# Kernel tuning notes

Hardware: AMD Instinct MI355X
Metric: run time of the kernel (lower is better)

Reference implementation:

```python
import jax, jax.numpy as jnp
import numpy as np

NEG = float(-2**32 + 1)  # padding value used by the original module
N_HEADS = 4


def setup_inputs() -> dict:
    key = jax.random.key(0)
    ks = jax.random.split(key, 12)
    B, L, H = 16, 200, 256
    queries = jax.random.normal(ks[0], (B, L, H), jnp.float32)
    keys = jax.random.normal(ks[1], (B, L, H), jnp.float32)
    time_mask = jax.random.randint(ks[2], (B, L), 0, 2) == 1
    attn_mask = jnp.triu(jnp.ones((L, L), dtype=bool), k=1)  # causal: True = masked
    time_matrix_K = jax.random.normal(ks[3], (B, L, L, H), jnp.float32) * 0.1
    time_matrix_V = jax.random.normal(ks[4], (B, L, L, H), jnp.float32) * 0.1
    abs_pos_K = jax.random.normal(ks[5], (B, L, H), jnp.float32)
    abs_pos_V = jax.random.normal(ks[6], (B, L, H), jnp.float32)
    s = 1.0 / np.sqrt(H)
    Wq = jax.random.normal(ks[7], (H, H), jnp.float32) * s
    Wk = jax.random.normal(ks[8], (H, H), jnp.float32) * s
    Wv = jax.random.normal(ks[9], (H, H), jnp.float32) * s
    bq = jnp.zeros((H,), jnp.float32)
    bk = jnp.zeros((H,), jnp.float32)
    bv = jnp.zeros((H,), jnp.float32)
    return dict(queries=queries, keys=keys, time_mask=time_mask, attn_mask=attn_mask,
                time_matrix_K=time_matrix_K, time_matrix_V=time_matrix_V,
                abs_pos_K=abs_pos_K, abs_pos_V=abs_pos_V,
                Wq=Wq, bq=bq, Wk=Wk, bk=bk, Wv=Wv, bv=bv)


def reference(queries, keys, time_mask, attn_mask, time_matrix_K, time_matrix_V,
              abs_pos_K, abs_pos_V, Wq, bq, Wk, bk, Wv, bv):
    B, L, H = queries.shape
    h = N_HEADS
    d = H // h
    # linear projections
    Q = (queries @ Wq.T + bq).reshape(B, L, h, d)
    K = (keys @ Wk.T + bk).reshape(B, L, h, d)
    V = (keys @ Wv.T + bv).reshape(B, L, h, d)
    posK = abs_pos_K.reshape(B, L, h, d)
    posV = abs_pos_V.reshape(B, L, h, d)
    tmK = time_matrix_K.reshape(B, L, L, h, d)
    tmV = time_matrix_V.reshape(B, L, L, h, d)
    # attention scores: content + absolute-position bias + per-row time bias
    scores = jnp.einsum('blhd,bmhd->bhlm', Q, K)
    scores += jnp.einsum('blhd,bmhd->bhlm', Q, posK)
    scores += jnp.einsum('blmhd,blhd->bhlm', tmK, Q)
    scores = scores / jnp.sqrt(jnp.asarray(d, scores.dtype))
    # time_mask masks query rows; attn_mask is causal [L,L]
    mask = time_mask[:, None, :, None] | attn_mask[None, None, :, :]  # [B,1,L,L]
    scores = jnp.where(mask, NEG, scores)
    A = jax.nn.softmax(scores, axis=-1)  # [B,h,L,L]; dropout_rate=0 -> identity
    out = jnp.einsum('bhlm,bmhd->blhd', A, V)
    out += jnp.einsum('bhlm,bmhd->blhd', A, posV)
    out += jnp.einsum('bhlm,blmhd->blhd', A, tmV)
    return out.reshape(B, L, H)
```

## Files before the change

kernel.cpp:

```cpp
#include <hip/hip_runtime.h>
#include <math.h>

#define LQ 200
#define HDIM 256

template <int CTRL>
__device__ __forceinline__ float dpp_add_step(float x) {
    int y = __builtin_amdgcn_update_dpp(0, __float_as_int(x), CTRL, 0xF, 0xF, true);
    return x + __int_as_float(y);
}
__device__ __forceinline__ float reduce16(float x) {
    x = dpp_add_step<0xB1>(x);
    x = dpp_add_step<0x4E>(x);
    x = dpp_add_step<0x141>(x);
    x = dpp_add_step<0x140>(x);
    return x;
}

__global__ __launch_bounds__(256) void proj_kernel(
    const float* __restrict__ queries, const float* __restrict__ keys,
    const float* __restrict__ posK, const float* __restrict__ posV,
    const float* __restrict__ Wq, const float* __restrict__ bq,
    const float* __restrict__ Wk, const float* __restrict__ bk,
    const float* __restrict__ Wv, const float* __restrict__ bv,
    float* __restrict__ Qp, float* __restrict__ Ksum, float* __restrict__ Vsum)
{
    __shared__ float qrow[8][HDIM];
    __shared__ float krow[8][HDIM];
    const int t = threadIdx.x;
    const int blk = blockIdx.x;
    const size_t base = (size_t)blk * 8 * HDIM;

    #pragma unroll
    for (int i = 0; i < 2; ++i) {
        int idx = i * 1024 + t * 4;
        *(float4*)&qrow[0][idx] = *(const float4*)&queries[base + idx];
        *(float4*)&krow[0][idx] = *(const float4*)&keys[base + idx];
    }
    __syncthreads();

    float accQ[8], accK[8], accV[8];
    #pragma unroll
    for (int r = 0; r < 8; ++r) { accQ[r] = 0.f; accK[r] = 0.f; accV[r] = 0.f; }

    const float4* wqp = (const float4*)&Wq[t * HDIM];
    const float4* wkp = (const float4*)&Wk[t * HDIM];
    const float4* wvp = (const float4*)&Wv[t * HDIM];

    for (int k4 = 0; k4 < HDIM / 4; ++k4) {
        float4 wq = wqp[k4], wk = wkp[k4], wv = wvp[k4];
        #pragma unroll
        for (int r = 0; r < 8; ++r) {
            float4 qv = *(const float4*)&qrow[r][k4 * 4];
            float4 kv = *(const float4*)&krow[r][k4 * 4];
            accQ[r] += qv.x * wq.x + qv.y * wq.y + qv.z * wq.z + qv.w * wq.w;
            accK[r] += kv.x * wk.x + kv.y * wk.y + kv.z * wk.z + kv.w * wk.w;
            accV[r] += kv.x * wv.x + kv.y * wv.y + kv.z * wv.z + kv.w * wv.w;
        }
    }

    const float bqv = bq[t], bkv = bk[t], bvv = bv[t];
    #pragma unroll
    for (int r = 0; r < 8; ++r) {
        size_t row = (size_t)blk * 8 + r;
        Qp[row * HDIM + t]   = (accQ[r] + bqv) * 0.125f;
        Ksum[row * HDIM + t] = accK[r] + bkv + posK[row * HDIM + t];
        Vsum[row * HDIM + t] = accV[r] + bvv + posV[row * HDIM + t];
    }
}

__global__ __launch_bounds__(256, 6) void attn_fused(
    const float* __restrict__ Qp, const float* __restrict__ Ksum,
    const float* __restrict__ Vsum, const float* __restrict__ tmK,
    const float* __restrict__ tmV, const int* __restrict__ tmask,
    float* __restrict__ out)
{
    __shared__ float outp[4][HDIM];
    __shared__ float Ssh[4][4];

    const int t = threadIdx.x;
    const int w = t >> 6;
    const int ln = t & 63;
    const int h = ln >> 4;
    const int c = ln * 4;
    const int blk = blockIdx.x;
    const int b = blk / LQ;
    const int l = blk - b * LQ;

    const bool rowmask = (tmask[blk] != 0);

    const float* pTV = tmV + (size_t)blk * (LQ * HDIM) + w * HDIM;
    const float* pVS = Vsum + (size_t)b * (LQ * HDIM) + w * HDIM;

    float4 acc = {0.f, 0.f, 0.f, 0.f};

    if (rowmask) {
        #pragma unroll 1
        for (int i = 0; i < LQ / 8; ++i) {
            const float4 a0 = *(const float4*)&pTV[c];
            const float4 b0 = *(const float4*)&pVS[c];
            const float4 a1 = *(const float4*)&pTV[4 * HDIM + c];
            const float4 b1 = *(const float4*)&pVS[4 * HDIM + c];
            acc.x += (a0.x + b0.x) + (a1.x + b1.x);
            acc.y += (a0.y + b0.y) + (a1.y + b1.y);
            acc.z += (a0.z + b0.z) + (a1.z + b1.z);
            acc.w += (a0.w + b0.w) + (a1.w + b1.w);
            pTV += 8 * HDIM;
            pVS += 8 * HDIM;
        }
        *(float4*)&outp[w][c] = acc;
        __syncthreads();
        out[(size_t)blk * HDIM + t] =
            (outp[0][t] + outp[1][t] + outp[2][t] + outp[3][t]) * (1.0f / LQ);
    } else {
        const float* pTK = tmK + (size_t)blk * (LQ * HDIM) + w * HDIM;
        const float* pKS = Ksum + (size_t)b * (LQ * HDIM) + w * HDIM;
        const float4 Q4 = *(const float4*)&Qp[(size_t)blk * HDIM + c];
        const int iters = (l >= w) ? ((l - w) >> 2) + 1 : 0;
        float S = 0.f;

        #pragma unroll 1
        for (int i = 0; i < iters; ++i) {
            const float4 k1 = *(const float4*)&pTK[c];
            const float4 k2 = *(const float4*)&pKS[c];
            const float4 v1 = *(const float4*)&pTV[c];
            const float4 v2 = *(const float4*)&pVS[c];
            float p = Q4.x * (k1.x + k2.x) + Q4.y * (k1.y + k2.y)
                    + Q4.z * (k1.z + k2.z) + Q4.w * (k1.w + k2.w);
            p = reduce16(p);
            const float e = __expf(p);
            acc.x += e * (v1.x + v2.x);
            acc.y += e * (v1.y + v2.y);
            acc.z += e * (v1.z + v2.z);
            acc.w += e * (v1.w + v2.w);
            S += e;
            pTK += 4 * HDIM;
            pKS += 4 * HDIM;
            pTV += 4 * HDIM;
            pVS += 4 * HDIM;
        }

        *(float4*)&outp[w][c] = acc;
        if ((ln & 15) == 0) Ssh[w][h] = S;
        __syncthreads();

        const int hh = t >> 6;
        const float Stot = Ssh[0][hh] + Ssh[1][hh] + Ssh[2][hh] + Ssh[3][hh];
        out[(size_t)blk * HDIM + t] =
            (outp[0][t] + outp[1][t] + outp[2][t] + outp[3][t]) / Stot;
    }
}

extern "C" void kernel_launch(void* const* d_in, const int* in_sizes, int n_in,
                              void* d_out, int out_size, void* d_ws, size_t ws_size,
                              hipStream_t stream) {
    const float* queries = (const float*)d_in[0];
    const float* keys    = (const float*)d_in[1];
    const int*   tmask   = (const int*)d_in[2];
    const float* tmK  = (const float*)d_in[4];
    const float* tmV  = (const float*)d_in[5];
    const float* posK = (const float*)d_in[6];
    const float* posV = (const float*)d_in[7];
    const float* Wq = (const float*)d_in[8];
    const float* bq = (const float*)d_in[9];
    const float* Wk = (const float*)d_in[10];
    const float* bk = (const float*)d_in[11];
    const float* Wv = (const float*)d_in[12];
    const float* bv = (const float*)d_in[13];

    float* ws   = (float*)d_ws;
    float* Qp   = ws;
    float* Ksum = ws + 819200;
    float* Vsum = ws + 2 * 819200;
    float* out  = (float*)d_out;

    hipLaunchKernelGGL(proj_kernel, dim3(400), dim3(256), 0, stream,
                       queries, keys, posK, posV, Wq, bq, Wk, bk, Wv, bv,
                       Qp, Ksum, Vsum);
    hipLaunchKernelGGL(attn_fused, dim3(3200), dim3(256), 0, stream,
                       Qp, Ksum, Vsum, tmK, tmV, tmask, out);
}
```

Before: 241.0 us.

## Software-pipeline attention loads and interleave block order across batches

Both attention loops now issue the loads for iteration i+1 before the arithmetic for iteration i, so memory latency is hidden within each wave. Blocks are remapped so that consecutive block IDs stride across batches, spreading the causal-row workload and HBM traffic more evenly. The occupancy hint of 6 in launch bounds is dropped, which lets the compiler use more registers for the extra in-flight loads but may lower occupancy.

```diff
diff --git a/kernel.cpp b/kernel.cpp
--- a/kernel.cpp
+++ b/kernel.cpp
@@ -69,7 +69,7 @@
     }
 }
 
-__global__ __launch_bounds__(256, 6) void attn_fused(
+__global__ __launch_bounds__(256) void attn_fused(
     const float* __restrict__ Qp, const float* __restrict__ Ksum,
     const float* __restrict__ Vsum, const float* __restrict__ tmK,
     const float* __restrict__ tmV, const int* __restrict__ tmask,
@@ -83,7 +83,8 @@
     const int ln = t & 63;
     const int h = ln >> 4;
     const int c = ln * 4;
-    const int blk = blockIdx.x;
+    const int bid = blockIdx.x;
+    const int blk = (bid & 7) * 400 + (bid >> 3);
     const int b = blk / LQ;
     const int l = blk - b * LQ;
 
@@ -95,19 +96,28 @@
     float4 acc = {0.f, 0.f, 0.f, 0.f};
 
     if (rowmask) {
-        #pragma unroll 1
-        for (int i = 0; i < LQ / 8; ++i) {
-            const float4 a0 = *(const float4*)&pTV[c];
-            const float4 b0 = *(const float4*)&pVS[c];
-            const float4 a1 = *(const float4*)&pTV[4 * HDIM + c];
-            const float4 b1 = *(const float4*)&pVS[4 * HDIM + c];
+        float4 a0 = *(const float4*)&pTV[c];
+        float4 b0 = *(const float4*)&pVS[c];
+        float4 a1 = *(const float4*)&pTV[4 * HDIM + c];
+        float4 b1 = *(const float4*)&pVS[4 * HDIM + c];
+        for (int i = 1; i < LQ / 8; ++i) {
+            pTV += 8 * HDIM;
+            pVS += 8 * HDIM;
+            const float4 na0 = *(const float4*)&pTV[c];
+            const float4 nb0 = *(const float4*)&pVS[c];
+            const float4 na1 = *(const float4*)&pTV[4 * HDIM + c];
+            const float4 nb1 = *(const float4*)&pVS[4 * HDIM + c];
             acc.x += (a0.x + b0.x) + (a1.x + b1.x);
             acc.y += (a0.y + b0.y) + (a1.y + b1.y);
             acc.z += (a0.z + b0.z) + (a1.z + b1.z);
             acc.w += (a0.w + b0.w) + (a1.w + b1.w);
-            pTV += 8 * HDIM;
-            pVS += 8 * HDIM;
+            a0 = na0; b0 = nb0; a1 = na1; b1 = nb1;
         }
+        acc.x += (a0.x + b0.x) + (a1.x + b1.x);
+        acc.y += (a0.y + b0.y) + (a1.y + b1.y);
+        acc.z += (a0.z + b0.z) + (a1.z + b1.z);
+        acc.w += (a0.w + b0.w) + (a1.w + b1.w);
+
         *(float4*)&outp[w][c] = acc;
         __syncthreads();
         out[(size_t)blk * HDIM + t] =
@@ -116,15 +126,32 @@
         const float* pTK = tmK + (size_t)blk * (LQ * HDIM) + w * HDIM;
         const float* pKS = Ksum + (size_t)b * (LQ * HDIM) + w * HDIM;
         const float4 Q4 = *(const float4*)&Qp[(size_t)blk * HDIM + c];
-        const int iters = (l >= w) ? ((l - w) >> 2) + 1 : 0;
+        const int n = (l >= w) ? ((l - w) >> 2) + 1 : 0;
         float S = 0.f;
 
-        #pragma unroll 1
-        for (int i = 0; i < iters; ++i) {
-            const float4 k1 = *(const float4*)&pTK[c];
-            const float4 k2 = *(const float4*)&pKS[c];
-            const float4 v1 = *(const float4*)&pTV[c];
-            const float4 v2 = *(const float4*)&pVS[c];
+        if (n > 0) {
+            float4 k1 = *(const float4*)&pTK[c];
+            float4 k2 = *(const float4*)&pKS[c];
+            float4 v1 = *(const float4*)&pTV[c];
+            float4 v2 = *(const float4*)&pVS[c];
+            for (int i = 1; i < n; ++i) {
+                pTK += 4 * HDIM; pKS += 4 * HDIM;
+                pTV += 4 * HDIM; pVS += 4 * HDIM;
+                const float4 nk1 = *(const float4*)&pTK[c];
+                const float4 nk2 = *(const float4*)&pKS[c];
+                const float4 nv1 = *(const float4*)&pTV[c];
+                const float4 nv2 = *(const float4*)&pVS[c];
+                float p = Q4.x * (k1.x + k2.x) + Q4.y * (k1.y + k2.y)
+                        + Q4.z * (k1.z + k2.z) + Q4.w * (k1.w + k2.w);
+                p = reduce16(p);
+                const float e = __expf(p);
+                acc.x += e * (v1.x + v2.x);
+                acc.y += e * (v1.y + v2.y);
+                acc.z += e * (v1.z + v2.z);
+                acc.w += e * (v1.w + v2.w);
+                S += e;
+                k1 = nk1; k2 = nk2; v1 = nv1; v2 = nv2;
+            }
             float p = Q4.x * (k1.x + k2.x) + Q4.y * (k1.y + k2.y)
                     + Q4.z * (k1.z + k2.z) + Q4.w * (k1.w + k2.w);
             p = reduce16(p);
@@ -134,10 +161,6 @@
             acc.z += e * (v1.z + v2.z);
             acc.w += e * (v1.w + v2.w);
             S += e;
-            pTK += 4 * HDIM;
-            pKS += 4 * HDIM;
-            pTV += 4 * HDIM;
-            pVS += 4 * HDIM;
         }
 
         *(float4*)&outp[w][c] = acc;
```

Result: no change. 236.6 us (-1.8%).

## Split attention into row-group column strips with LDS-shared K/V and combine pass

Applied to the files above, without the earlier changes.

The per-row attention kernel becomes a split-K design. Each block handles 8 query rows over one of 5 column strips of 40 keys, and the Ksum/Vsum tiles are double-buffered in LDS so all 8 rows share them. Unnormalized partial accumulators and softmax sums go to workspace, and a new combine kernel adds the strips and normalizes. The aims are more independent loads in flight per wave, less repeated Ksum/Vsum traffic, and better load balance across the causal triangle. The cost is an extra kernel launch and extra partial-sum traffic through global memory.

```diff
diff --git a/kernel.cpp b/kernel.cpp
--- a/kernel.cpp
+++ b/kernel.cpp
@@ -3,6 +3,11 @@
 
 #define LQ 200
 #define HDIM 256
+#define G 8
+#define NSTRIP 5
+#define SLEN 40
+#define NCHUNK 10
+#define NROW 3200
 
 template <int CTRL>
 __device__ __forceinline__ float dpp_add_step(float x) {
@@ -69,86 +74,126 @@
     }
 }
 
-__global__ __launch_bounds__(256, 6) void attn_fused(
+__global__ __launch_bounds__(256) void attn_part(
     const float* __restrict__ Qp, const float* __restrict__ Ksum,
     const float* __restrict__ Vsum, const float* __restrict__ tmK,
     const float* __restrict__ tmV, const int* __restrict__ tmask,
-    float* __restrict__ out)
+    float* __restrict__ pacc, float* __restrict__ pS)
 {
-    __shared__ float outp[4][HDIM];
-    __shared__ float Ssh[4][4];
+    __shared__ float ks[2][4][HDIM];
+    __shared__ float vs[2][4][HDIM];
 
     const int t = threadIdx.x;
     const int w = t >> 6;
     const int ln = t & 63;
-    const int h = ln >> 4;
     const int c = ln * 4;
-    const int blk = blockIdx.x;
-    const int b = blk / LQ;
-    const int l = blk - b * LQ;
-
-    const bool rowmask = (tmask[blk] != 0);
-
-    const float* pTV = tmV + (size_t)blk * (LQ * HDIM) + w * HDIM;
-    const float* pVS = Vsum + (size_t)b * (LQ * HDIM) + w * HDIM;
-
-    float4 acc = {0.f, 0.f, 0.f, 0.f};
-
-    if (rowmask) {
-        #pragma unroll 1
-        for (int i = 0; i < LQ / 8; ++i) {
-            const float4 a0 = *(const float4*)&pTV[c];
-            const float4 b0 = *(const float4*)&pVS[c];
-            const float4 a1 = *(const float4*)&pTV[4 * HDIM + c];
-            const float4 b1 = *(const float4*)&pVS[4 * HDIM + c];
-            acc.x += (a0.x + b0.x) + (a1.x + b1.x);
-            acc.y += (a0.y + b0.y) + (a1.y + b1.y);
-            acc.z += (a0.z + b0.z) + (a1.z + b1.z);
-            acc.w += (a0.w + b0.w) + (a1.w + b1.w);
-            pTV += 8 * HDIM;
-            pVS += 8 * HDIM;
+    const int bid = blockIdx.x;
+    const int blk = (bid & 7) * 250 + (bid >> 3);
+    const int g = blk / NSTRIP;
+    const int s = blk - g * NSTRIP;
+    const int b = g / 25;
+    const int l0 = (g - b * 25) * G;
+    const int m0 = s * SLEN;
+
+    const int r0 = l0 + 2 * w;
+    const int r1 = r0 + 1;
+    const size_t rowsz = (size_t)LQ * HDIM;
+    const float* KS = Ksum + (size_t)b * rowsz;
+    const float* VS = Vsum + (size_t)b * rowsz;
+    const float* tK0 = tmK + ((size_t)(b * LQ + r0)) * rowsz;
+    const float* tV0 = tmV + ((size_t)(b * LQ + r0)) * rowsz;
+    const float* tK1 = tmK + ((size_t)(b * LQ + r1)) * rowsz;
+    const float* tV1 = tmV + ((size_t)(b * LQ + r1)) * rowsz;
+    const bool mask0 = (tmask[b * LQ + r0] != 0);
+    const bool mask1 = (tmask[b * LQ + r1] != 0);
+    const float4 Q0 = *(const float4*)&Qp[((size_t)(b * LQ + r0)) * HDIM + c];
+    const float4 Q1 = *(const float4*)&Qp[((size_t)(b * LQ + r1)) * HDIM + c];
+
+    float4 acc0 = {0.f, 0.f, 0.f, 0.f}, acc1 = {0.f, 0.f, 0.f, 0.f};
+    float S0 = 0.f, S1 = 0.f;
+
+    auto stage = [&](int buf, int ch) {
+        const size_t mo = (size_t)(m0 + ch * 4 + w) * HDIM + c;
+        const float4 kq = *(const float4*)&KS[mo];
+        const float4 vq = *(const float4*)&VS[mo];
+        *(float4*)&ks[buf][w][c] = kq;
+        *(float4*)&vs[buf][w][c] = vq;
+    };
+
+    stage(0, 0);
+    __syncthreads();
+
+    for (int ch = 0; ch < NCHUNK; ++ch) {
+        const int cur = ch & 1;
+        if (ch + 1 < NCHUNK) stage(cur ^ 1, ch + 1);
+
+        #pragma unroll
+        for (int mm = 0; mm < 4; ++mm) {
+            const int m = m0 + ch * 4 + mm;
+            if (mask0 || m <= r0) {
+                const float4 v1 = *(const float4*)&tV0[(size_t)m * HDIM + c];
+                const float4 vsm = *(const float4*)&vs[cur][mm][c];
+                float e;
+                if (!mask0) {
+                    const float4 k1 = *(const float4*)&tK0[(size_t)m * HDIM + c];
+                    const float4 ksm = *(const float4*)&ks[cur][mm][c];
+                    float p = Q0.x * (k1.x + ksm.x) + Q0.y * (k1.y + ksm.y)
+                            + Q0.z * (k1.z + ksm.z) + Q0.w * (k1.w + ksm.w);
+                    p = reduce16(p);
+                    e = __expf(p);
+                } else e = 1.0f;
+                acc0.x += e * (v1.x + vsm.x);
+                acc0.y += e * (v1.y + vsm.y);
+                acc0.z += e * (v1.z + vsm.z);
+                acc0.w += e * (v1.w + vsm.w);
+                S0 += e;
+            }
+            if (mask1 || m <= r1) {
+                const float4 v1 = *(const float4*)&tV1[(size_t)m * HDIM + c];
+                const float4 vsm = *(const float4*)&vs[cur][mm][c];
+                float e;
+                if (!mask1) {
+                    const float4 k1 = *(const float4*)&tK1[(size_t)m * HDIM + c];
+                    const float4 ksm = *(const float4*)&ks[cur][mm][c];
+                    float p = Q1.x * (k1.x + ksm.x) + Q1.y * (k1.y + ksm.y)
+                            + Q1.z * (k1.z + ksm.z) + Q1.w * (k1.w + ksm.w);
+                    p = reduce16(p);
+                    e = __expf(p);
+                } else e = 1.0f;
+                acc1.x += e * (v1.x + vsm.x);
+                acc1.y += e * (v1.y + vsm.y);
+                acc1.z += e * (v1.z + vsm.z);
+                acc1.w += e * (v1.w + vsm.w);
+                S1 += e;
+            }
         }
-        *(float4*)&outp[w][c] = acc;
         __syncthreads();
-        out[(size_t)blk * HDIM + t] =
-            (outp[0][t] + outp[1][t] + outp[2][t] + outp[3][t]) * (1.0f / LQ);
-    } else {
-        const float* pTK = tmK + (size_t)blk * (LQ * HDIM) + w * HDIM;
-        const float* pKS = Ksum + (size_t)b * (LQ * HDIM) + w * HDIM;
-        const float4 Q4 = *(const float4*)&Qp[(size_t)blk * HDIM + c];
-        const int iters = (l >= w) ? ((l - w) >> 2) + 1 : 0;
-        float S = 0.f;
-
-        #pragma unroll 1
-        for (int i = 0; i < iters; ++i) {
-            const float4 k1 = *(const float4*)&pTK[c];
-            const float4 k2 = *(const float4*)&pKS[c];
-            const float4 v1 = *(const float4*)&pTV[c];
-            const float4 v2 = *(const float4*)&pVS[c];
-            float p = Q4.x * (k1.x + k2.x) + Q4.y * (k1.y + k2.y)
-                    + Q4.z * (k1.z + k2.z) + Q4.w * (k1.w + k2.w);
-            p = reduce16(p);
-            const float e = __expf(p);
-            acc.x += e * (v1.x + v2.x);
-            acc.y += e * (v1.y + v2.y);
-            acc.z += e * (v1.z + v2.z);
-            acc.w += e * (v1.w + v2.w);
-            S += e;
-            pTK += 4 * HDIM;
-            pKS += 4 * HDIM;
-            pTV += 4 * HDIM;
-            pVS += 4 * HDIM;
-        }
-
-        *(float4*)&outp[w][c] = acc;
-        if ((ln & 15) == 0) Ssh[w][h] = S;
-        __syncthreads();
-
-        const int hh = t >> 6;
-        const float Stot = Ssh[0][hh] + Ssh[1][hh] + Ssh[2][hh] + Ssh[3][hh];
-        out[(size_t)blk * HDIM + t] =
-            (outp[0][t] + outp[1][t] + outp[2][t] + outp[3][t]) / Stot;
-    }
+    }
+
+    const int row0 = b * LQ + r0;
+    const int row1 = b * LQ + r1;
+    *(float4*)&pacc[((size_t)s * NROW + row0) * HDIM + c] = acc0;
+    *(float4*)&pacc[((size_t)s * NROW + row1) * HDIM + c] = acc1;
+    if ((ln & 15) == 0) {
+        pS[((size_t)s * NROW + row0) * 4 + (ln >> 4)] = S0;
+        pS[((size_t)s * NROW + row1) * 4 + (ln >> 4)] = S1;
+    }
+}
+
+__global__ __launch_bounds__(256) void combine_kernel(
+    const float* __restrict__ pacc, const float* __restrict__ pS,
+    float* __restrict__ out)
+{
+    const int row = blockIdx.x;
+    const int t = threadIdx.x;
+    const int h = t >> 6;
+    float a = 0.f, S = 0.f;
+    #pragma unroll
+    for (int s = 0; s < NSTRIP; ++s) {
+        a += pacc[((size_t)s * NROW + row) * HDIM + t];
+        S += pS[((size_t)s * NROW + row) * 4 + h];
+    }
+    out[(size_t)row * HDIM + t] = a / S;
 }
 
 extern "C" void kernel_launch(void* const* d_in, const int* in_sizes, int n_in,
@@ -172,11 +217,15 @@
     float* Qp   = ws;
     float* Ksum = ws + 819200;
     float* Vsum = ws + 2 * 819200;
+    float* pacc = ws + 3 * 819200;
+    float* pS   = pacc + (size_t)NSTRIP * NROW * HDIM;
     float* out  = (float*)d_out;
 
     hipLaunchKernelGGL(proj_kernel, dim3(400), dim3(256), 0, stream,
                        queries, keys, posK, posV, Wq, bq, Wk, bk, Wv, bv,
                        Qp, Ksum, Vsum);
-    hipLaunchKernelGGL(attn_fused, dim3(3200), dim3(256), 0, stream,
-                       Qp, Ksum, Vsum, tmK, tmV, tmask, out);
-}
+    hipLaunchKernelGGL(attn_part, dim3(400 * NSTRIP), dim3(256), 0, stream,
+                       Qp, Ksum, Vsum, tmK, tmV, tmask, pacc, pS);
+    hipLaunchKernelGGL(combine_kernel, dim3(NROW), dim3(256), 0, stream,
+                       pacc, pS, out);
+}
```

Result: faster. 230.6 us (-4.3%).

## Stage time-matrix rows into LDS via async global_load_lds double buffering

Applied to the files above, without the earlier changes.

The attention kernel now copies tmK/tmV rows into shared memory in 8-key chunks with global_load_lds, double-buffering so the next chunk loads while the current one is consumed. The masked-row and causal paths are merged into one loop that uses e=1 for masked rows. The aim is to hide global-memory latency on the large time-matrix stream. In exchange it adds a barrier per chunk and about 36KB of shared memory per block, and drops the occupancy hint of 6 blocks, which may cut resident blocks per CU.

```diff
diff --git a/kernel.cpp b/kernel.cpp
--- a/kernel.cpp
+++ b/kernel.cpp
@@ -3,6 +3,13 @@
 
 #define LQ 200
 #define HDIM 256
+#define CHK 8
+
+__device__ __forceinline__ void gload_lds16(const float* g, float* l) {
+    __builtin_amdgcn_global_load_lds(
+        (const __attribute__((address_space(1))) void*)g,
+        (__attribute__((address_space(3))) void*)l, 16, 0, 0);
+}
 
 template <int CTRL>
 __device__ __forceinline__ float dpp_add_step(float x) {
@@ -69,12 +76,14 @@
     }
 }
 
-__global__ __launch_bounds__(256, 6) void attn_fused(
+__global__ __launch_bounds__(256) void attn_dma(
     const float* __restrict__ Qp, const float* __restrict__ Ksum,
     const float* __restrict__ Vsum, const float* __restrict__ tmK,
     const float* __restrict__ tmV, const int* __restrict__ tmask,
     float* __restrict__ out)
 {
+    __shared__ float kt[2][CHK][HDIM];
+    __shared__ float vt[2][CHK][HDIM];
     __shared__ float outp[4][HDIM];
     __shared__ float Ssh[4][4];
 
@@ -88,67 +97,72 @@
     const int l = blk - b * LQ;
 
     const bool rowmask = (tmask[blk] != 0);
+    const size_t rowsz = (size_t)LQ * HDIM;
+    const float* tVr = tmV + (size_t)blk * rowsz;
+    const float* tKr = tmK + (size_t)blk * rowsz;
+    const float* KS  = Ksum + (size_t)b * rowsz;
+    const float* VS  = Vsum + (size_t)b * rowsz;
+    const int nkeys = rowmask ? LQ : (l + 1);
+    const int nch = (nkeys + CHK - 1) / CHK;
 
-    const float* pTV = tmV + (size_t)blk * (LQ * HDIM) + w * HDIM;
-    const float* pVS = Vsum + (size_t)b * (LQ * HDIM) + w * HDIM;
+    const float4 Q4 = *(const float4*)&Qp[(size_t)blk * HDIM + c];
+
+    auto stage = [&](int buf, int ch) {
+        const int j0 = 2 * w;
+        const size_t base = (size_t)(ch * CHK) * HDIM + (size_t)ln * 4;
+        gload_lds16(tVr + base + (size_t)j0 * HDIM,       &vt[buf][j0][0]);
+        gload_lds16(tVr + base + (size_t)(j0 + 1) * HDIM, &vt[buf][j0 + 1][0]);
+        if (!rowmask) {
+            gload_lds16(tKr + base + (size_t)j0 * HDIM,       &kt[buf][j0][0]);
+            gload_lds16(tKr + base + (size_t)(j0 + 1) * HDIM, &kt[buf][j0 + 1][0]);
+        }
+    };
 
     float4 acc = {0.f, 0.f, 0.f, 0.f};
+    float S = 0.f;
 
-    if (rowmask) {
-        #pragma unroll 1
-        for (int i = 0; i < LQ / 8; ++i) {
-            const float4 a0 = *(const float4*)&pTV[c];
-            const float4 b0 = *(const float4*)&pVS[c];
-            const float4 a1 = *(const float4*)&pTV[4 * HDIM + c];
-            const float4 b1 = *(const float4*)&pVS[4 * HDIM + c];
-            acc.x += (a0.x + b0.x) + (a1.x + b1.x);
-            acc.y += (a0.y + b0.y) + (a1.y + b1.y);
-            acc.z += (a0.z + b0.z) + (a1.z + b1.z);
-            acc.w += (a0.w + b0.w) + (a1.w + b1.w);
-            pTV += 8 * HDIM;
-            pVS += 8 * HDIM;
+    stage(0, 0);
+    __syncthreads();
+    int cur = 0;
+    for (int ch = 0; ch < nch; ++ch) {
+        if (ch + 1 < nch) stage(cur ^ 1, ch + 1);
+        #pragma unroll
+        for (int q = 0; q < 2; ++q) {
+            const int mm = w + 4 * q;
+            const int m = ch * CHK + mm;
+            if (m < nkeys) {
+                const float4 v1 = *(const float4*)&vt[cur][mm][c];
+                const float4 v2 = *(const float4*)&VS[(size_t)m * HDIM + c];
+                float e;
+                if (rowmask) {
+                    e = 1.0f;
+                } else {
+                    const float4 k1 = *(const float4*)&kt[cur][mm][c];
+                    const float4 k2 = *(const float4*)&KS[(size_t)m * HDIM + c];
+                    float p = Q4.x * (k1.x + k2.x) + Q4.y * (k1.y + k2.y)
+                            + Q4.z * (k1.z + k2.z) + Q4.w * (k1.w + k2.w);
+                    p = reduce16(p);
+                    e = __expf(p);
+                }
+                acc.x += e * (v1.x + v2.x);
+                acc.y += e * (v1.y + v2.y);
+                acc.z += e * (v1.z + v2.z);
+                acc.w += e * (v1.w + v2.w);
+                S += e;
+            }
         }
-        *(float4*)&outp[w][c] = acc;
         __syncthreads();
-        out[(size_t)blk * HDIM + t] =
-            (outp[0][t] + outp[1][t] + outp[2][t] + outp[3][t]) * (1.0f / LQ);
-    } else {
-        const float* pTK = tmK + (size_t)blk * (LQ * HDIM) + w * HDIM;
-        const float* pKS = Ksum + (size_t)b * (LQ * HDIM) + w * HDIM;
-        const float4 Q4 = *(const float4*)&Qp[(size_t)blk * HDIM + c];
-        const int iters = (l >= w) ? ((l - w) >> 2) + 1 : 0;
-        float S = 0.f;
+        cur ^= 1;
+    }
 
-        #pragma unroll 1
-        for (int i = 0; i < iters; ++i) {
-            const float4 k1 = *(const float4*)&pTK[c];
-            const float4 k2 = *(const float4*)&pKS[c];
-            const float4 v1 = *(const float4*)&pTV[c];
-            const float4 v2 = *(const float4*)&pVS[c];
-            float p = Q4.x * (k1.x + k2.x) + Q4.y * (k1.y + k2.y)
-                    + Q4.z * (k1.z + k2.z) + Q4.w * (k1.w + k2.w);
-            p = reduce16(p);
-            const float e = __expf(p);
-            acc.x += e * (v1.x + v2.x);
-            acc.y += e * (v1.y + v2.y);
-            acc.z += e * (v1.z + v2.z);
-            acc.w += e * (v1.w + v2.w);
-            S += e;
-            pTK += 4 * HDIM;
-            pKS += 4 * HDIM;
-            pTV += 4 * HDIM;
-            pVS += 4 * HDIM;
-        }
+    *(float4*)&outp[w][c] = acc;
+    if ((ln & 15) == 0) Ssh[w][h] = S;
+    __syncthreads();
 
-        *(float4*)&outp[w][c] = acc;
-        if ((ln & 15) == 0) Ssh[w][h] = S;
-        __syncthreads();
-
-        const int hh = t >> 6;
-        const float Stot = Ssh[0][hh] + Ssh[1][hh] + Ssh[2][hh] + Ssh[3][hh];
-        out[(size_t)blk * HDIM + t] =
-            (outp[0][t] + outp[1][t] + outp[2][t] + outp[3][t]) / Stot;
-    }
+    const int hh = t >> 6;
+    const float Stot = Ssh[0][hh] + Ssh[1][hh] + Ssh[2][hh] + Ssh[3][hh];
+    out[(size_t)blk * HDIM + t] =
+        (outp[0][t] + outp[1][t] + outp[2][t] + outp[3][t]) / Stot;
 }
 
 extern "C" void kernel_launch(void* const* d_in, const int* in_sizes, int n_in,
@@ -177,6 +191,6 @@
     hipLaunchKernelGGL(proj_kernel, dim3(400), dim3(256), 0, stream,
                        queries, keys, posK, posV, Wq, bq, Wk, bk, Wv, bv,
                        Qp, Ksum, Vsum);
-    hipLaunchKernelGGL(attn_fused, dim3(3200), dim3(256), 0, stream,
+    hipLaunchKernelGGL(attn_dma, dim3(3200), dim3(256), 0, stream,
                        Qp, Ksum, Vsum, tmK, tmV, tmask, out);
 }
```

Result: no change. 245.2 us (+1.8%).
